# Kernel optimization log

Hardware: AMD Instinct MI355X
Metric: run time of the kernel (lower is better)

## Reference

```python
import jax, jax.numpy as jnp
import numpy as np

N, E, L, D, H, NC = 50000, 400000, 1024, 256, 4, 2
C = D // H  # per-head dim


def setup_inputs() -> dict:
    key = jax.random.key(0)
    ks = jax.random.split(key, 12)
    s = 1.0 / np.sqrt(L)
    sd = 1.0 / np.sqrt(D)
    return {
        "x": jax.random.normal(ks[0], (N, L), dtype=jnp.float32),
        "edge_index": jax.random.randint(ks[1], (2, E), 0, N, dtype=jnp.int32),
        "label": 1,
        "Wq": jax.random.normal(ks[2], (L, D), dtype=jnp.float32) * s,
        "bq": jnp.zeros((D,), dtype=jnp.float32),
        "Wk": jax.random.normal(ks[3], (L, D), dtype=jnp.float32) * s,
        "bk": jnp.zeros((D,), dtype=jnp.float32),
        "Wv": jax.random.normal(ks[4], (L, D), dtype=jnp.float32) * s,
        "bv": jnp.zeros((D,), dtype=jnp.float32),
        "Wskip": jax.random.normal(ks[5], (L, D), dtype=jnp.float32) * s,
        "bskip": jnp.zeros((D,), dtype=jnp.float32),
        "gate_w": jax.random.normal(ks[6], (D, NC), dtype=jnp.float32) * sd,
        "gate_b": jnp.zeros((NC,), dtype=jnp.float32),
        "pool_w": jax.random.normal(ks[7], (D, D), dtype=jnp.float32) * sd,
        "pool_b": jnp.zeros((D,), dtype=jnp.float32),
    }


def reference(x, edge_index, label, Wq, bq, Wk, bk, Wv, bv, Wskip, bskip,
              gate_w, gate_b, pool_w, pool_b):
    src, dst = edge_index[0], edge_index[1]
    # per-head projections [N, H, C]
    q = (x @ Wq + bq).reshape(N, H, C)
    k = (x @ Wk + bk).reshape(N, H, C)
    v = (x @ Wv + bv).reshape(N, H, C)
    # edge attention scores, softmax over incoming edges per destination node
    s = jnp.einsum('ehc,ehc->eh', q[dst], k[src]) / np.sqrt(C)  # [E, H]
    m = jax.ops.segment_max(s, dst, num_segments=N)             # [N, H]
    ex = jnp.exp(s - m[dst])
    den = jax.ops.segment_sum(ex, dst, num_segments=N)          # [N, H]
    alpha = ex / den[dst]                                       # [E, H]
    agg = jax.ops.segment_sum(alpha[:, :, None] * v[src], dst,
                              num_segments=N).reshape(N, D)
    h = agg + x @ Wskip + bskip                                 # root/skip term
    h = jax.nn.gelu(h, approximate=False)
    # global adaptive attention pooling: per-class softmax over nodes
    scores = h @ gate_w + gate_b                                # [N, NC]
    attn = jax.nn.softmax(scores, axis=0)                       # [N, NC]
    y = jnp.einsum('nc,nd->cd', attn, h @ pool_w + pool_b)      # [NC, D]
    A = attn[:, label]
    return (y, attn, h, A)
```

## Files before the change

kernel.cpp:

```cpp
#include <hip/hip_runtime.h>
#include <stdint.h>

#define N_NODES 50000
#define N_EDGES 400000
#define M_PAD   50048

typedef __attribute__((ext_vector_type(8))) __bf16 bf16x8;
typedef __attribute__((ext_vector_type(4))) float floatx4;

__device__ __forceinline__ unsigned short f2bf(float f) {
    unsigned int u = __float_as_uint(f);
    unsigned int r = (u + 0x7fffu + ((u >> 16) & 1u)) >> 16;
    return (unsigned short)r;
}

__device__ __forceinline__ void gload_lds16(const void* g, void* l) {
    __builtin_amdgcn_global_load_lds((__attribute__((address_space(1))) void*)g,
                                     (__attribute__((address_space(3))) void*)l,
                                     16, 0, 0);
}

__global__ void k_conv_x(const float* __restrict__ x, unsigned short* __restrict__ xb) {
    const int total = M_PAD * 256;
    for (int u = blockIdx.x * blockDim.x + threadIdx.x; u < total; u += gridDim.x * blockDim.x) {
        int row = u >> 8;
        int c4  = u & 255;
        float4 v = make_float4(0.f, 0.f, 0.f, 0.f);
        if (row < N_NODES) v = ((const float4*)x)[(size_t)row * 256 + c4];
        ushort4 o;
        o.x = f2bf(v.x); o.y = f2bf(v.y); o.z = f2bf(v.z); o.w = f2bf(v.w);
        ((ushort4*)xb)[u] = o;
    }
}

__global__ void k_build_w(const float* __restrict__ Wq, const float* __restrict__ Wk,
                          const float* __restrict__ Wv, const float* __restrict__ Ws,
                          const float* __restrict__ bq, const float* __restrict__ bk,
                          const float* __restrict__ bv, const float* __restrict__ bs,
                          unsigned short* __restrict__ WT, float* __restrict__ biascat) {
    int idx = blockIdx.x * blockDim.x + threadIdx.x;
    if (idx < 1024 * 1024) {
        int n = idx >> 10;
        int k = idx & 1023;
        int g = n >> 8, d = n & 255;
        const float* W = (g == 0) ? Wq : (g == 1) ? Wk : (g == 2) ? Wv : Ws;
        WT[idx] = f2bf(W[k * 256 + d]);
    }
    if (idx < 1024) {
        int g = idx >> 8, d = idx & 255;
        const float* B = (g == 0) ? bq : (g == 1) ? bk : (g == 2) ? bv : bs;
        biascat[idx] = B[d];
    }
}

__launch_bounds__(256)
__global__ void k_gemm(const unsigned short* __restrict__ A,
                       const unsigned short* __restrict__ BT,
                       const float* __restrict__ bias,
                       float* __restrict__ Cmat) {
    __shared__ unsigned short As[128 * 32];
    __shared__ unsigned short Bs[128 * 32];
    const int t = threadIdx.x;
    const int w = t >> 6;
    const int l = t & 63;
    const int row0 = blockIdx.y * 128;
    const int col0 = blockIdx.x * 128;

    const int lr = l >> 2;
    const int lc = (l & 3) * 8;

    const int wr = (w >> 1) * 64;
    const int wc = (w & 1) * 64;
    const int lane15 = l & 15;
    const int quad = l >> 4;

    floatx4 acc[4][4];
#pragma unroll
    for (int i = 0; i < 4; i++)
#pragma unroll
        for (int j = 0; j < 4; j++) acc[i][j] = (floatx4)0.f;

    for (int kk = 0; kk < 1024; kk += 32) {
        __syncthreads();
#pragma unroll
        for (int issue = 0; issue < 2; issue++) {
            int arow = row0 + issue * 64 + w * 16 + lr;
            gload_lds16(A + (size_t)arow * 1024 + kk + lc, As + issue * 2048 + w * 512);
            int brow = col0 + issue * 64 + w * 16 + lr;
            gload_lds16(BT + (size_t)brow * 1024 + kk + lc, Bs + issue * 2048 + w * 512);
        }
        __builtin_amdgcn_s_waitcnt(0x0f70);
        __syncthreads();

        bf16x8 af[4], bfr[4];
#pragma unroll
        for (int i = 0; i < 4; i++) {
            af[i]  = *(const bf16x8*)(As + (wr + i * 16 + lane15) * 32 + quad * 8);
            bfr[i] = *(const bf16x8*)(Bs + (wc + i * 16 + lane15) * 32 + quad * 8);
        }
#pragma unroll
        for (int i = 0; i < 4; i++)
#pragma unroll
            for (int j = 0; j < 4; j++)
                acc[i][j] = __builtin_amdgcn_mfma_f32_16x16x32_bf16(af[i], bfr[j], acc[i][j], 0, 0, 0);
    }

#pragma unroll
    for (int i = 0; i < 4; i++) {
#pragma unroll
        for (int j = 0; j < 4; j++) {
            int col = col0 + wc + j * 16 + lane15;
            float bcol = bias[col];
#pragma unroll
            for (int r = 0; r < 4; r++) {
                int row = row0 + wr + i * 16 + quad * 4 + r;
                Cmat[(size_t)row * 1024 + col] = acc[i][j][r] + bcol;
            }
        }
    }
}

__global__ void k_hist(const int* __restrict__ ei, int* __restrict__ cnt) {
    int e = blockIdx.x * blockDim.x + threadIdx.x;
    if (e >= N_EDGES) return;
    atomicAdd(&cnt[ei[N_EDGES + e]], 1);
}

__global__ void k_scan(const int* __restrict__ cnt, int* __restrict__ offs) {
    __shared__ int wsums[4];
    const int CH = 196;
    int t = threadIdx.x;
    int beg = t * CH;
    int end = beg + CH; if (end > N_NODES) end = N_NODES;
    int s = 0;
    for (int i = beg; i < end; i++) s += cnt[i];
    int lane = t & 63, w = t >> 6;
    int v = s;
#pragma unroll
    for (int off = 1; off < 64; off <<= 1) {
        int u = __shfl_up(v, off, 64);
        if (lane >= off) v += u;
    }
    if (lane == 63) wsums[w] = v;
    __syncthreads();
    int carry = 0;
    for (int i = 0; i < w; i++) carry += wsums[i];
    int run = carry + v - s;
    for (int i = beg; i < end; i++) {
        offs[i] = run;
        run += cnt[i];
    }
    if (t == 255) offs[N_NODES] = run;
}

__global__ void k_scatter(const int* __restrict__ ei, const int* __restrict__ offs,
                          int* __restrict__ fill, int* __restrict__ ssrc) {
    int e = blockIdx.x * blockDim.x + threadIdx.x;
    if (e >= N_EDGES) return;
    int src = ei[e];
    int dst = ei[N_EDGES + e];
    int pos = offs[dst] + atomicAdd(&fill[dst], 1);
    ssrc[pos] = src;
}

__launch_bounds__(256)
__global__ void k_attn(const int* __restrict__ offs, const int* __restrict__ ssrc,
                       const float* __restrict__ qkvs,
                       const float* __restrict__ gate_w, const float* __restrict__ gate_b,
                       float* __restrict__ out_h, float* __restrict__ exsc) {
    int w = threadIdx.x >> 6, l = threadIdx.x & 63;
    int n = blockIdx.x * 4 + w;
    if (n >= N_NODES) return;

    float4 qv = ((const float4*)(qkvs + (size_t)n * 1024))[l];
    int beg = offs[n], end = offs[n + 1];

    float4 acc = make_float4(0.f, 0.f, 0.f, 0.f);
    float den = 0.f;

    for (int base = beg; base < end; base += 64) {
        int m = end - base; if (m > 64) m = 64;
        int mysrc = (l < m) ? ssrc[base + l] : 0;
#pragma unroll 2
        for (int j = 0; j < m; j++) {
            int src = __shfl(mysrc, j, 64);
            const float* row = qkvs + (size_t)src * 1024;
            float4 kv = ((const float4*)(row + 256))[l];
            float4 vv = ((const float4*)(row + 512))[l];
            float p = qv.x * kv.x + qv.y * kv.y + qv.z * kv.z + qv.w * kv.w;
            p += __shfl_xor(p, 1, 16);
            p += __shfl_xor(p, 2, 16);
            p += __shfl_xor(p, 4, 16);
            p += __shfl_xor(p, 8, 16);
            float ex = expf(p * 0.125f);
            den += ex;
            acc.x += ex * vv.x; acc.y += ex * vv.y;
            acc.z += ex * vv.z; acc.w += ex * vv.w;
        }
    }

    float inv = (den > 0.f) ? 1.f / den : 0.f;
    float4 sk = ((const float4*)(qkvs + (size_t)n * 1024 + 768))[l];

    float z0 = acc.x * inv + sk.x;
    float z1 = acc.y * inv + sk.y;
    float z2 = acc.z * inv + sk.z;
    float z3 = acc.w * inv + sk.w;

    const float is2 = 0.70710678118f;
    float h0 = 0.5f * z0 * (1.f + erff(z0 * is2));
    float h1 = 0.5f * z1 * (1.f + erff(z1 * is2));
    float h2 = 0.5f * z2 * (1.f + erff(z2 * is2));
    float h3 = 0.5f * z3 * (1.f + erff(z3 * is2));
    ((float4*)(out_h + (size_t)n * 256))[l] = make_float4(h0, h1, h2, h3);

    int d0 = l * 4;
    float s0 = h0 * gate_w[(d0 + 0) * 2] + h1 * gate_w[(d0 + 1) * 2] +
               h2 * gate_w[(d0 + 2) * 2] + h3 * gate_w[(d0 + 3) * 2];
    float s1 = h0 * gate_w[(d0 + 0) * 2 + 1] + h1 * gate_w[(d0 + 1) * 2 + 1] +
               h2 * gate_w[(d0 + 2) * 2 + 1] + h3 * gate_w[(d0 + 3) * 2 + 1];
#pragma unroll
    for (int off = 1; off < 64; off <<= 1) {
        s0 += __shfl_xor(s0, off, 64);
        s1 += __shfl_xor(s1, off, 64);
    }
    if (l == 0) {
        exsc[n * 2 + 0] = expf(s0 + gate_b[0]);
        exsc[n * 2 + 1] = expf(s1 + gate_b[1]);
    }
}

__global__ void k_esum(const float* __restrict__ exsc, float* __restrict__ esum) {
    __shared__ float red0[4], red1[4];
    float p0 = 0.f, p1 = 0.f;
    for (int n = blockIdx.x * blockDim.x + threadIdx.x; n < N_NODES; n += gridDim.x * blockDim.x) {
        p0 += exsc[n * 2];
        p1 += exsc[n * 2 + 1];
    }
#pragma unroll
    for (int off = 1; off < 64; off <<= 1) {
        p0 += __shfl_xor(p0, off, 64);
        p1 += __shfl_xor(p1, off, 64);
    }
    int w = threadIdx.x >> 6, l = threadIdx.x & 63;
    if (l == 0) { red0[w] = p0; red1[w] = p1; }
    __syncthreads();
    if (threadIdx.x == 0) {
        atomicAdd(&esum[0], red0[0] + red0[1] + red0[2] + red0[3]);
        atomicAdd(&esum[1], red1[0] + red1[1] + red1[2] + red1[3]);
    }
}

__global__ void k_t(const float* __restrict__ exsc, const float* __restrict__ esum,
                    const float* __restrict__ h_f, const int* __restrict__ label_p,
                    float* __restrict__ attn_out, float* __restrict__ A_out,
                    float* __restrict__ t_ws) {
    int d = threadIdx.x;
    float inv0 = 1.f / esum[0], inv1 = 1.f / esum[1];
    int lab = *label_p;
    int n0 = blockIdx.x * 98;
    int n1 = n0 + 98; if (n1 > N_NODES) n1 = N_NODES;
    float t0 = 0.f, t1 = 0.f;
    for (int n = n0; n < n1; n++) {
        float e0 = exsc[n * 2], e1 = exsc[n * 2 + 1];
        float a0 = e0 * inv0, a1 = e1 * inv1;
        float hv = h_f[(size_t)n * 256 + d];
        t0 += a0 * hv;
        t1 += a1 * hv;
        if (d == 0) attn_out[n * 2] = a0;
        else if (d == 1) attn_out[n * 2 + 1] = a1;
        else if (d == 2) A_out[n] = (lab == 0) ? a0 : a1;
    }
    atomicAdd(&t_ws[d], t0);
    atomicAdd(&t_ws[256 + d], t1);
}

__global__ void k_y(const float* __restrict__ t_ws, const float* __restrict__ pool_w,
                    const float* __restrict__ pool_b, float* __restrict__ y_out) {
    int d = threadIdx.x;
    float a0 = pool_b[d], a1 = pool_b[d];
    for (int k = 0; k < 256; k++) {
        float w = pool_w[k * 256 + d];
        a0 += t_ws[k] * w;
        a1 += t_ws[256 + k] * w;
    }
    y_out[d] = a0;
    y_out[256 + d] = a1;
}

extern "C" void kernel_launch(void* const* d_in, const int* in_sizes, int n_in,
                              void* d_out, int out_size, void* d_ws, size_t ws_size,
                              hipStream_t stream) {
    const float* x      = (const float*)d_in[0];
    const int*   ei     = (const int*)d_in[1];
    const int*   label  = (const int*)d_in[2];
    const float* Wq     = (const float*)d_in[3];
    const float* bq     = (const float*)d_in[4];
    const float* Wk     = (const float*)d_in[5];
    const float* bk     = (const float*)d_in[6];
    const float* Wv     = (const float*)d_in[7];
    const float* bv     = (const float*)d_in[8];
    const float* Wskip  = (const float*)d_in[9];
    const float* bskip  = (const float*)d_in[10];
    const float* gate_w = (const float*)d_in[11];
    const float* gate_b = (const float*)d_in[12];
    const float* pool_w = (const float*)d_in[13];
    const float* pool_b = (const float*)d_in[14];

    char* ws = (char*)d_ws;
    size_t off = 0;
    float* qkvs = (float*)(ws + off);                 off += (size_t)M_PAD * 1024 * 4;
    unsigned short* xb = (unsigned short*)(ws + off); off += (size_t)M_PAD * 1024 * 2;
    unsigned short* WT = (unsigned short*)(ws + off); off += (size_t)1024 * 1024 * 2;
    float* biascat = (float*)(ws + off);              off += 1024 * 4;
    int* cnt  = (int*)(ws + off);                     off += (size_t)N_NODES * 4;
    int* fill = (int*)(ws + off);                     off += (size_t)N_NODES * 4;
    int* offs = (int*)(ws + off);                     off += (size_t)(N_NODES + 1) * 4;
    int* ssrc = (int*)(ws + off);                     off += (size_t)N_EDGES * 4;
    float* exsc = (float*)(ws + off);                 off += (size_t)N_NODES * 2 * 4;
    float* esum = (float*)(ws + off);                 off += 2 * 4;
    float* t_ws = (float*)(ws + off);                 off += 512 * 4;

    float* out = (float*)d_out;
    float* y_out    = out;
    float* attn_out = out + 512;
    float* h_out    = out + 100512;
    float* A_out    = out + 12900512;

    hipMemsetAsync(cnt, 0, (size_t)N_NODES * 2 * 4, stream);
    hipMemsetAsync(esum, 0, (2 + 512) * 4, stream);

    k_conv_x<<<4096, 256, 0, stream>>>(x, xb);
    k_build_w<<<4096, 256, 0, stream>>>(Wq, Wk, Wv, Wskip, bq, bk, bv, bskip, WT, biascat);
    k_hist<<<(N_EDGES + 255) / 256, 256, 0, stream>>>(ei, cnt);
    k_scan<<<1, 256, 0, stream>>>(cnt, offs);
    k_scatter<<<(N_EDGES + 255) / 256, 256, 0, stream>>>(ei, offs, fill, ssrc);
    dim3 ggrid(8, 391);
    k_gemm<<<ggrid, 256, 0, stream>>>(xb, WT, biascat, qkvs);
    k_attn<<<12500, 256, 0, stream>>>(offs, ssrc, qkvs, gate_w, gate_b, h_out, exsc);
    k_esum<<<128, 256, 0, stream>>>(exsc, esum);
    k_t<<<512, 256, 0, stream>>>(exsc, esum, h_out, label, attn_out, A_out, t_ws);
    k_y<<<1, 256, 0, stream>>>(t_ws, pool_w, pool_b, y_out);
}
```

Baseline: 841.3 us.

## Double-buffer GEMM LDS tiles and remap blocks for XCD-aware locality

The GEMM kernel now double-buffers its A/B shared-memory tiles, prefetching the next K-slice while MFMAs run on the current one, which cuts one barrier per iteration. The 2D grid is replaced by a 1D grid that maps workgroups so that each XCD's consecutive blocks share row tiles, aiming for better L2 reuse of the A operand. This doubles LDS use per block, which may lower occupancy, and 3136 blocks with early-exit leaves some blocks idle.

After: 836.2 us. About the same (-0.6%).

```diff
diff --git a/kernel.cpp b/kernel.cpp
--- a/kernel.cpp
+++ b/kernel.cpp
@@ -58,13 +58,23 @@
                        const unsigned short* __restrict__ BT,
                        const float* __restrict__ bias,
                        float* __restrict__ Cmat) {
-    __shared__ unsigned short As[128 * 32];
-    __shared__ unsigned short Bs[128 * 32];
+    __shared__ unsigned short As[2 * 128 * 32];
+    __shared__ unsigned short Bs[2 * 128 * 32];
+
+    int wg   = blockIdx.x;
+    int xcd  = wg & 7;
+    int j    = wg >> 3;
+    int xt   = j & 7;
+    int ygrp = j >> 3;
+    int yt   = ygrp * 8 + xcd;
+    if (yt >= 391) return;
+
+    const int row0 = yt * 128;
+    const int col0 = xt * 128;
+
     const int t = threadIdx.x;
     const int w = t >> 6;
     const int l = t & 63;
-    const int row0 = blockIdx.y * 128;
-    const int col0 = blockIdx.x * 128;
 
     const int lr = l >> 2;
     const int lc = (l & 3) * 8;
@@ -78,43 +88,60 @@
 #pragma unroll
     for (int i = 0; i < 4; i++)
 #pragma unroll
-        for (int j = 0; j < 4; j++) acc[i][j] = (floatx4)0.f;
-
-    for (int kk = 0; kk < 1024; kk += 32) {
-        __syncthreads();
+        for (int j2 = 0; j2 < 4; j2++) acc[i][j2] = (floatx4)0.f;
+
+    auto stage = [&](int buf, int kk) {
+        unsigned short* Ab = As + buf * 4096;
+        unsigned short* Bb = Bs + buf * 4096;
 #pragma unroll
         for (int issue = 0; issue < 2; issue++) {
             int arow = row0 + issue * 64 + w * 16 + lr;
-            gload_lds16(A + (size_t)arow * 1024 + kk + lc, As + issue * 2048 + w * 512);
+            gload_lds16(A + (size_t)arow * 1024 + kk + lc, Ab + issue * 2048 + w * 512);
             int brow = col0 + issue * 64 + w * 16 + lr;
-            gload_lds16(BT + (size_t)brow * 1024 + kk + lc, Bs + issue * 2048 + w * 512);
-        }
-        __builtin_amdgcn_s_waitcnt(0x0f70);
-        __syncthreads();
-
+            gload_lds16(BT + (size_t)brow * 1024 + kk + lc, Bb + issue * 2048 + w * 512);
+        }
+    };
+
+    const int NK = 1024 / 32;
+
+    stage(0, 0);
+    __builtin_amdgcn_s_waitcnt(0x0f70);
+    __syncthreads();
+
+    for (int step = 0; step < NK; ++step) {
+        int cur = step & 1;
+        if (step + 1 < NK) stage(cur ^ 1, (step + 1) * 32);
+
+        const unsigned short* Ab = As + cur * 4096;
+        const unsigned short* Bb = Bs + cur * 4096;
         bf16x8 af[4], bfr[4];
 #pragma unroll
         for (int i = 0; i < 4; i++) {
-            af[i]  = *(const bf16x8*)(As + (wr + i * 16 + lane15) * 32 + quad * 8);
-            bfr[i] = *(const bf16x8*)(Bs + (wc + i * 16 + lane15) * 32 + quad * 8);
+            af[i]  = *(const bf16x8*)(Ab + (wr + i * 16 + lane15) * 32 + quad * 8);
+            bfr[i] = *(const bf16x8*)(Bb + (wc + i * 16 + lane15) * 32 + quad * 8);
         }
 #pragma unroll
         for (int i = 0; i < 4; i++)
 #pragma unroll
-            for (int j = 0; j < 4; j++)
-                acc[i][j] = __builtin_amdgcn_mfma_f32_16x16x32_bf16(af[i], bfr[j], acc[i][j], 0, 0, 0);
+            for (int j2 = 0; j2 < 4; j2++)
+                acc[i][j2] = __builtin_amdgcn_mfma_f32_16x16x32_bf16(af[i], bfr[j2], acc[i][j2], 0, 0, 0);
+
+        if (step + 1 < NK) {
+            __builtin_amdgcn_s_waitcnt(0x0f70);
+            __syncthreads();
+        }
     }
 
 #pragma unroll
     for (int i = 0; i < 4; i++) {
 #pragma unroll
-        for (int j = 0; j < 4; j++) {
-            int col = col0 + wc + j * 16 + lane15;
+        for (int j2 = 0; j2 < 4; j2++) {
+            int col = col0 + wc + j2 * 16 + lane15;
             float bcol = bias[col];
 #pragma unroll
             for (int r = 0; r < 4; r++) {
                 int row = row0 + wr + i * 16 + quad * 4 + r;
-                Cmat[(size_t)row * 1024 + col] = acc[i][j][r] + bcol;
+                Cmat[(size_t)row * 1024 + col] = acc[i][j2][r] + bcol;
             }
         }
     }
@@ -335,8 +362,7 @@
     k_hist<<<(N_EDGES + 255) / 256, 256, 0, stream>>>(ei, cnt);
     k_scan<<<1, 256, 0, stream>>>(cnt, offs);
     k_scatter<<<(N_EDGES + 255) / 256, 256, 0, stream>>>(ei, offs, fill, ssrc);
-    dim3 ggrid(8, 391);
-    k_gemm<<<ggrid, 256, 0, stream>>>(xb, WT, biascat, qkvs);
+    k_gemm<<<3136, 256, 0, stream>>>(xb, WT, biascat, qkvs);
     k_attn<<<12500, 256, 0, stream>>>(offs, ssrc, qkvs, gate_w, gate_b, h_out, exsc);
     k_esum<<<128, 256, 0, stream>>>(exsc, esum);
     k_t<<<512, 256, 0, stream>>>(exsc, esum, h_out, label, attn_out, A_out, t_ws);
```

## Restructure QKV GEMM into 256x256 tiles with multi-stage LDS pipeline

Applied to the files above, without the earlier changes.

Rewrites the fused projection GEMM to use 256x256 output tiles per 512-thread workgroup, with a 4-buffer LDS ring for A prefetched two k-steps ahead. B fragments now load straight from global memory into registers, double-buffered. It also adds an XOR swizzle against LDS bank conflicts, a workgroup index remap for cache locality, and raised MFMA priority. Row padding grows to a multiple of 256. The aim is more reuse per tile and overlap of loads with MFMA, at the cost of more registers (128 accumulator values per thread) and some padded work.

Result: slower. 866.9 us (+3.0%).

```diff
diff --git a/kernel.cpp b/kernel.cpp
--- a/kernel.cpp
+++ b/kernel.cpp
@@ -3,7 +3,7 @@
 
 #define N_NODES 50000
 #define N_EDGES 400000
-#define M_PAD   50048
+#define M_PAD   50176
 
 typedef __attribute__((ext_vector_type(8))) __bf16 bf16x8;
 typedef __attribute__((ext_vector_type(4))) float floatx4;
@@ -53,68 +53,110 @@
     }
 }
 
-__launch_bounds__(256)
+__launch_bounds__(512, 2)
 __global__ void k_gemm(const unsigned short* __restrict__ A,
                        const unsigned short* __restrict__ BT,
                        const float* __restrict__ bias,
                        float* __restrict__ Cmat) {
-    __shared__ unsigned short As[128 * 32];
-    __shared__ unsigned short Bs[128 * 32];
+    __shared__ unsigned short As[4 * 8192];
+
+    const int wg  = blockIdx.x;
+    const int idx = (wg & 7) * 98 + (wg >> 3);
+    const int yt  = idx >> 2;
+    const int xt  = idx & 3;
+    const int row0 = yt * 256;
+    const int col0 = xt * 256;
+
     const int t = threadIdx.x;
     const int w = t >> 6;
     const int l = t & 63;
-    const int row0 = blockIdx.y * 128;
-    const int col0 = blockIdx.x * 128;
-
-    const int lr = l >> 2;
-    const int lc = (l & 3) * 8;
-
-    const int wr = (w >> 1) * 64;
-    const int wc = (w & 1) * 64;
     const int lane15 = l & 15;
-    const int quad = l >> 4;
-
-    floatx4 acc[4][4];
-#pragma unroll
-    for (int i = 0; i < 4; i++)
-#pragma unroll
-        for (int j = 0; j < 4; j++) acc[i][j] = (floatx4)0.f;
-
-    for (int kk = 0; kk < 1024; kk += 32) {
-        __syncthreads();
-#pragma unroll
-        for (int issue = 0; issue < 2; issue++) {
-            int arow = row0 + issue * 64 + w * 16 + lr;
-            gload_lds16(A + (size_t)arow * 1024 + kk + lc, As + issue * 2048 + w * 512);
-            int brow = col0 + issue * 64 + w * 16 + lr;
-            gload_lds16(BT + (size_t)brow * 1024 + kk + lc, Bs + issue * 2048 + w * 512);
-        }
-        __builtin_amdgcn_s_waitcnt(0x0f70);
-        __syncthreads();
-
-        bf16x8 af[4], bfr[4];
-#pragma unroll
-        for (int i = 0; i < 4; i++) {
-            af[i]  = *(const bf16x8*)(As + (wr + i * 16 + lane15) * 32 + quad * 8);
-            bfr[i] = *(const bf16x8*)(Bs + (wc + i * 16 + lane15) * 32 + quad * 8);
-        }
-#pragma unroll
-        for (int i = 0; i < 4; i++)
-#pragma unroll
-            for (int j = 0; j < 4; j++)
-                acc[i][j] = __builtin_amdgcn_mfma_f32_16x16x32_bf16(af[i], bfr[j], acc[i][j], 0, 0, 0);
-    }
-
-#pragma unroll
-    for (int i = 0; i < 4; i++) {
-#pragma unroll
-        for (int j = 0; j < 4; j++) {
-            int col = col0 + wc + j * 16 + lane15;
+    const int quad   = l >> 4;
+
+    const int wr = (w >> 2) * 128;
+    const int wc = (w & 3) * 64;
+
+    const int qx   = quad ^ ((lane15 >> 1) & 3);
+    const int qsrc = (l & 3) ^ ((l >> 3) & 3);
+    const int srow = w * 16 + (l >> 2);
+
+    unsigned short* Asl = As;
+
+    floatx4 acc[8][4];
+#pragma unroll
+    for (int i = 0; i < 8; i++)
+#pragma unroll
+        for (int c = 0; c < 4; c++) acc[i][c] = (floatx4)0.f;
+
+#define ASTAGE(buf, ktn)                                                                  \
+    {                                                                                     \
+        const size_t kko = (size_t)(ktn) * 32;                                            \
+        _Pragma("unroll")                                                                 \
+        for (int h = 0; h < 2; h++) {                                                     \
+            int rowg = h * 128 + srow;                                                    \
+            gload_lds16(A + (size_t)(row0 + rowg) * 1024 + kko + qsrc * 8,                \
+                        Asl + (size_t)(buf) * 8192 + (h * 512 + w * 64) * 8);             \
+        }                                                                                 \
+    }
+
+#define BPREF(BARR, ktn)                                                                  \
+    {                                                                                     \
+        const size_t kko = (size_t)(ktn) * 32;                                            \
+        _Pragma("unroll")                                                                 \
+        for (int c = 0; c < 4; c++)                                                       \
+            BARR[c] = *(const bf16x8*)(BT + (size_t)(col0 + wc + c * 16 + lane15) * 1024  \
+                                          + kko + quad * 8);                              \
+    }
+
+#define TILE(kt, BCUR, BNXT)                                                              \
+    {                                                                                     \
+        if ((kt) + 1 < 32) BPREF(BNXT, (kt) + 1);                                         \
+        if ((kt) + 2 < 32) ASTAGE(((kt) + 2) & 3, (kt) + 2);                              \
+        const unsigned short* Ab = Asl + (size_t)((kt) & 3) * 8192;                       \
+        bf16x8 af[8];                                                                     \
+        _Pragma("unroll")                                                                 \
+        for (int i = 0; i < 8; i++)                                                       \
+            af[i] = *(const bf16x8*)(Ab + (wr + i * 16 + lane15) * 32 + qx * 8);          \
+        __builtin_amdgcn_s_setprio(1);                                                    \
+        _Pragma("unroll")                                                                 \
+        for (int i = 0; i < 8; i++)                                                       \
+            _Pragma("unroll")                                                             \
+            for (int c = 0; c < 4; c++)                                                   \
+                acc[i][c] = __builtin_amdgcn_mfma_f32_16x16x32_bf16(af[i], BCUR[c],       \
+                                                                   acc[i][c], 0, 0, 0);  \
+        __builtin_amdgcn_s_setprio(0);                                                    \
+        if ((kt) < 30)       __builtin_amdgcn_s_waitcnt(0x0f76);            \
+        else if ((kt) == 30) __builtin_amdgcn_s_waitcnt(0x0f74);            \
+        if ((kt) < 31) __syncthreads();                                                   \
+    }
+
+    bf16x8 bA[4], bB[4];
+
+    ASTAGE(0, 0);
+    ASTAGE(1, 1);
+    BPREF(bA, 0);
+    __builtin_amdgcn_s_waitcnt(0x0f76);
+    __syncthreads();
+
+    for (int kt = 0; kt < 32; kt += 2) {
+        TILE(kt, bA, bB);
+        TILE(kt + 1, bB, bA);
+    }
+
+#undef TILE
+#undef BPREF
+#undef ASTAGE
+
+#pragma unroll
+    for (int i = 0; i < 8; i++) {
+#pragma unroll
+        for (int c = 0; c < 4; c++) {
+            int col = col0 + wc + c * 16 + lane15;
             float bcol = bias[col];
 #pragma unroll
             for (int r = 0; r < 4; r++) {
                 int row = row0 + wr + i * 16 + quad * 4 + r;
-                Cmat[(size_t)row * 1024 + col] = acc[i][j][r] + bcol;
+                Cmat[(size_t)row * 1024 + col] = acc[i][c][r] + bcol;
             }
         }
     }
@@ -335,8 +377,7 @@
     k_hist<<<(N_EDGES + 255) / 256, 256, 0, stream>>>(ei, cnt);
     k_scan<<<1, 256, 0, stream>>>(cnt, offs);
     k_scatter<<<(N_EDGES + 255) / 256, 256, 0, stream>>>(ei, offs, fill, ssrc);
-    dim3 ggrid(8, 391);
-    k_gemm<<<ggrid, 256, 0, stream>>>(xb, WT, biascat, qkvs);
+    k_gemm<<<784, 512, 0, stream>>>(xb, WT, biascat, qkvs);
     k_attn<<<12500, 256, 0, stream>>>(offs, ssrc, qkvs, gate_w, gate_b, h_out, exsc);
     k_esum<<<128, 256, 0, stream>>>(exsc, esum);
     k_t<<<512, 256, 0, stream>>>(exsc, esum, h_out, label, attn_out, A_out, t_ws);
```
